# Performance work log

Hardware: AMD Instinct MI355X
Metric: run time of the kernel (lower is better)

Reference implementation:

```python
import jax, jax.numpy as jnp
import numpy as np

B = 524288        # batch
W = 64            # window_size


def setup_inputs() -> dict:
    key = jax.random.key(0)
    k1, k2, k3 = jax.random.split(key, 3)
    x = jax.random.normal(k1, (B, W), dtype=jnp.float32)
    theta = 0.01 * jax.random.normal(k2, (W, 2), dtype=jnp.float32)
    w = jax.random.normal(k3, (1, 1), dtype=jnp.float32)
    b = jnp.zeros((1,), dtype=jnp.float32)
    return {"x": x, "theta": theta, "w": w, "b": b}


def _expval_z(x, theta):
    """Single-qubit re-uploading circuit: for each t, RX(x_t) RY(th_t0) RZ(th_t1)
    applied to |0>, then <Z>. State carried as two complex amplitudes [B]."""
    bsz = x.shape[0]
    s0 = jnp.ones((bsz,), dtype=jnp.complex64)
    s1 = jnp.zeros((bsz,), dtype=jnp.complex64)

    def step(state, inp):
        s0, s1 = state
        xt, th = inp                      # xt: [B], th: [2]
        # RX(xt): [[c, -i s], [-i s, c]], half-angle
        c = jnp.cos(0.5 * xt).astype(jnp.complex64)
        s = jnp.sin(0.5 * xt).astype(jnp.complex64)
        n0 = c * s0 - 1j * s * s1
        n1 = -1j * s * s0 + c * s1
        # RY(th[0]): [[cy, -sy], [sy, cy]]
        cy = jnp.cos(0.5 * th[0]).astype(jnp.complex64)
        sy = jnp.sin(0.5 * th[0]).astype(jnp.complex64)
        m0 = cy * n0 - sy * n1
        m1 = sy * n0 + cy * n1
        # RZ(th[1]): diag(e^{-i th/2}, e^{+i th/2})
        p = jnp.exp(-0.5j * th[1].astype(jnp.complex64))
        return (p * m0, jnp.conj(p) * m1), None

    (s0, s1), _ = jax.lax.scan(step, (s0, s1), (x.T, theta))  # xs leading dim W
    # <Z> = |s0|^2 - |s1|^2 (real)
    return ((s0 * jnp.conj(s0) - s1 * jnp.conj(s1)).real).astype(jnp.float32)


def reference(x, theta, w, b):
    z = _expval_z(x, theta)               # [B]
    return z * w[0, 0] + b[0]             # Linear(1,1) readout, squeezed -> [B]
```

## Files before the change

kernel.cpp:

```cpp
#include <hip/hip_runtime.h>

#define WSZ    64
#define BLOCK  64
#define INV2PI 0.15915494309189535f

__global__ __launch_bounds__(BLOCK) void sq_main(
    const float* __restrict__ x,
    const float* __restrict__ theta,
    const float* __restrict__ w,
    const float* __restrict__ bias,
    float* __restrict__ out)
{
    __shared__ float4 xs4[WSZ * 16];
    __shared__ float4 tA[WSZ];
    __shared__ float4 tB[WSZ];

    const int tid = threadIdx.x;
    const size_t row0 = (size_t)blockIdx.x * BLOCK;
    const float* xblk = x + row0 * WSZ;

#if defined(__has_builtin) && __has_builtin(__builtin_amdgcn_global_load_lds)
    #pragma unroll
    for (int i = 0; i < 16; ++i) {
        int row = i * 4 + (tid >> 4);
        int c4  = (tid & 15) ^ (row & 7);
        const float* src = xblk + row * WSZ + c4 * 4;
        __builtin_amdgcn_global_load_lds(
            (const __attribute__((address_space(1))) void*)src,
            (__attribute__((address_space(3))) void*)&xs4[i * 64], 16, 0, 0);
    }
#else
    #pragma unroll
    for (int i = 0; i < 16; ++i) {
        int row = i * 4 + (tid >> 4);
        int c4  = (tid & 15) ^ (row & 7);
        xs4[i * 64 + tid] = *reinterpret_cast<const float4*>(xblk + row * WSZ + c4 * 4);
    }
#endif

    {
        float a = theta[2 * tid + 0] * INV2PI;
        float b = theta[2 * tid + 1] * INV2PI;
        float sa = __builtin_amdgcn_sinf(a), ca = __builtin_amdgcn_cosf(a);
        float sb = __builtin_amdgcn_sinf(b), cb = __builtin_amdgcn_cosf(b);
        tA[tid] = make_float4(cb * ca, -sb, cb * sa, sb * ca);
        tB[tid] = make_float4(cb, sb * sa, -sa, ca);
    }

    __syncthreads();

    float vx = 0.0f, vy = 0.0f, vz = 1.0f;
    const int rbase = tid * 16;
    const int rx    = tid & 7;

    #pragma unroll
    for (int c = 0; c < 16; ++c) {
        float4 xv = xs4[rbase + (c ^ rx)];
        #pragma unroll
        for (int j = 0; j < 4; ++j) {
            const int t = c * 4 + j;
            float r  = ((const float*)&xv)[j] * INV2PI;
            float s  = __builtin_amdgcn_sinf(r);
            float co = __builtin_amdgcn_cosf(r);
            float4 A  = tA[t];
            float4 Bv = tB[t];
            float y1 = co * vy - s * vz;
            float z1 = s  * vy + co * vz;
            float nx = A.x  * vx + A.y  * y1 + A.z  * z1;
            float ny = A.w  * vx + Bv.x * y1 + Bv.y * z1;
            float nz = Bv.z * vx + Bv.w * z1;
            vx = nx; vy = ny; vz = nz;
        }
    }

    out[row0 + tid] = vz * w[0] + bias[0];
}

extern "C" void kernel_launch(void* const* d_in, const int* in_sizes, int n_in,
                              void* d_out, int out_size, void* d_ws, size_t ws_size,
                              hipStream_t stream) {
    const float* x     = (const float*)d_in[0];
    const float* theta = (const float*)d_in[1];
    const float* w     = (const float*)d_in[2];
    const float* b     = (const float*)d_in[3];
    float* out = (float*)d_out;

    int nrows = out_size;
    int grid  = nrows / BLOCK;
    sq_main<<<grid, BLOCK, 0, stream>>>(x, theta, w, b, out);
}
```

Baseline: 38.80 us.

## Double-buffer per-wave x loads into LDS and broadcast theta via readlane

Restructures the kernel so each wavefront independently streams its 64 rows of x into LDS in four column quarters with double buffering, using vmcnt waits instead of a block-wide barrier so loads overlap the rotation math. The per-timestep rotation matrix entries are now held in registers (one timestep per lane) and broadcast with readlane rather than read from shared memory. The block grows to four waves. It relies on hand-placed s_waitcnt counts matching the compiler's load ordering and on the absence of cross-lane LDS hazards, since there is no barrier between the async LDS writes and the reads.

```diff
diff --git a/kernel.cpp b/kernel.cpp
--- a/kernel.cpp
+++ b/kernel.cpp
@@ -1,8 +1,15 @@
 #include <hip/hip_runtime.h>
 
 #define WSZ    64
-#define BLOCK  64
+#define BLOCK  256
 #define INV2PI 0.15915494309189535f
+
+#define VM_WAIT4 asm volatile("s_waitcnt vmcnt(4)" ::: "memory")
+#define VM_WAIT0 asm volatile("s_waitcnt vmcnt(0)" ::: "memory")
+
+__device__ __forceinline__ float rl(float v, int t) {
+    return __builtin_bit_cast(float, __builtin_amdgcn_readlane(__builtin_bit_cast(int, v), t));
+}
 
 __global__ __launch_bounds__(BLOCK) void sq_main(
     const float* __restrict__ x,
@@ -11,69 +18,78 @@
     const float* __restrict__ bias,
     float* __restrict__ out)
 {
-    __shared__ float4 xs4[WSZ * 16];
-    __shared__ float4 tA[WSZ];
-    __shared__ float4 tB[WSZ];
+    __shared__ float4 xs4[4][2][256];
 
-    const int tid = threadIdx.x;
-    const size_t row0 = (size_t)blockIdx.x * BLOCK;
-    const float* xblk = x + row0 * WSZ;
+    const int tid  = threadIdx.x;
+    const int lane = tid & 63;
+    const int wid  = tid >> 6;
+    const size_t wrow0 = (size_t)blockIdx.x * BLOCK + wid * 64;
+    const float* xw = x + wrow0 * WSZ;
 
-#if defined(__has_builtin) && __has_builtin(__builtin_amdgcn_global_load_lds)
-    #pragma unroll
-    for (int i = 0; i < 16; ++i) {
-        int row = i * 4 + (tid >> 4);
-        int c4  = (tid & 15) ^ (row & 7);
-        const float* src = xblk + row * WSZ + c4 * 4;
-        __builtin_amdgcn_global_load_lds(
-            (const __attribute__((address_space(1))) void*)src,
-            (__attribute__((address_space(3))) void*)&xs4[i * 64], 16, 0, 0);
-    }
-#else
-    #pragma unroll
-    for (int i = 0; i < 16; ++i) {
-        int row = i * 4 + (tid >> 4);
-        int c4  = (tid & 15) ^ (row & 7);
-        xs4[i * 64 + tid] = *reinterpret_cast<const float4*>(xblk + row * WSZ + c4 * 4);
-    }
-#endif
+    float4* buf0 = &xs4[wid][0][0];
+    float4* buf1 = &xs4[wid][1][0];
 
-    {
-        float a = theta[2 * tid + 0] * INV2PI;
-        float b = theta[2 * tid + 1] * INV2PI;
-        float sa = __builtin_amdgcn_sinf(a), ca = __builtin_amdgcn_cosf(a);
-        float sb = __builtin_amdgcn_sinf(b), cb = __builtin_amdgcn_cosf(b);
-        tA[tid] = make_float4(cb * ca, -sb, cb * sa, sb * ca);
-        tB[tid] = make_float4(cb, sb * sa, -sa, ca);
-    }
+    float2 th = reinterpret_cast<const float2*>(theta)[lane];
+    float sa = __builtin_amdgcn_sinf(th.x * INV2PI);
+    float ca = __builtin_amdgcn_cosf(th.x * INV2PI);
+    float sb = __builtin_amdgcn_sinf(th.y * INV2PI);
+    float cb = __builtin_amdgcn_cosf(th.y * INV2PI);
+    float m00 = cb * ca, m01 = -sb,     m02 = cb * sa;
+    float m10 = sb * ca, m11 = cb,      m12 = sb * sa;
+    float m20 = -sa,     m22 = ca;
 
-    __syncthreads();
+    auto issue = [&](int q, float4* buf) {
+        #pragma unroll
+        for (int i = 0; i < 4; ++i) {
+            int l    = i * 64 + lane;
+            int row  = l >> 2;
+            int cl   = l & 3;
+            int cg   = cl ^ ((row >> 1) & 3);
+            const float* src = xw + (size_t)row * WSZ + q * 16 + cg * 4;
+            __builtin_amdgcn_global_load_lds(
+                (const __attribute__((address_space(1))) void*)src,
+                (__attribute__((address_space(3))) void*)&buf[i * 64], 16, 0, 0);
+        }
+    };
 
     float vx = 0.0f, vy = 0.0f, vz = 1.0f;
-    const int rbase = tid * 16;
-    const int rx    = tid & 7;
+    const int key = (lane >> 1) & 3;
 
-    #pragma unroll
-    for (int c = 0; c < 16; ++c) {
-        float4 xv = xs4[rbase + (c ^ rx)];
+    auto quarter = [&](int q, const float4* buf) {
         #pragma unroll
-        for (int j = 0; j < 4; ++j) {
-            const int t = c * 4 + j;
-            float r  = ((const float*)&xv)[j] * INV2PI;
-            float s  = __builtin_amdgcn_sinf(r);
-            float co = __builtin_amdgcn_cosf(r);
-            float4 A  = tA[t];
-            float4 Bv = tB[t];
-            float y1 = co * vy - s * vz;
-            float z1 = s  * vy + co * vz;
-            float nx = A.x  * vx + A.y  * y1 + A.z  * z1;
-            float ny = A.w  * vx + Bv.x * y1 + Bv.y * z1;
-            float nz = Bv.z * vx + Bv.w * z1;
-            vx = nx; vy = ny; vz = nz;
+        for (int c = 0; c < 4; ++c) {
+            float4 xv = buf[lane * 4 + (c ^ key)];
+            float xr[4] = {xv.x, xv.y, xv.z, xv.w};
+            #pragma unroll
+            for (int j = 0; j < 4; ++j) {
+                const int t = q * 16 + c * 4 + j;
+                float r  = xr[j] * INV2PI;
+                float s  = __builtin_amdgcn_sinf(r);
+                float co = __builtin_amdgcn_cosf(r);
+                float y1 = co * vy - s * vz;
+                float z1 = s  * vy + co * vz;
+                float nx = rl(m00,t) * vx + rl(m01,t) * y1 + rl(m02,t) * z1;
+                float ny = rl(m10,t) * vx + rl(m11,t) * y1 + rl(m12,t) * z1;
+                float nz = rl(m20,t) * vx + rl(m22,t) * z1;
+                vx = nx; vy = ny; vz = nz;
+            }
         }
-    }
+    };
 
-    out[row0 + tid] = vz * w[0] + bias[0];
+    issue(0, buf0);
+    issue(1, buf1);
+    VM_WAIT4;
+    quarter(0, buf0);
+    issue(2, buf0);
+    VM_WAIT4;
+    quarter(1, buf1);
+    issue(3, buf1);
+    VM_WAIT4;
+    quarter(2, buf0);
+    VM_WAIT0;
+    quarter(3, buf1);
+
+    out[wrow0 + lane] = vz * w[0] + bias[0];
 }
 
 extern "C" void kernel_launch(void* const* d_in, const int* in_sizes, int n_in,
```

Measured after the change: 42.00 us. 1.08x slower.
